# Optimization experiments

Measured on AMD Instinct MI355X. Metric: run time of the kernel, lower is better.

Reference implementation:

```python
import jax, jax.numpy as jnp
import numpy as np

BITS = 4
GROUP = 128
IN_F = 4096
OUT_F = 11008
N_GROUPS = IN_F // GROUP  # padded_in == in_features here


def fwht(v):
    """Orthonormal fast Walsh-Hadamard transform over the last axis (len = power of 2)."""
    orig = v.shape
    g = orig[-1]
    x = v.reshape(-1, g)
    h = 1
    while h < g:
        x = x.reshape(-1, g // (2 * h), 2, h)
        a, b = x[:, :, 0, :], x[:, :, 1, :]
        x = jnp.stack([a + b, a - b], axis=2).reshape(-1, g)
        h *= 2
    return (x * (1.0 / np.sqrt(g))).reshape(orig)


def setup_inputs() -> dict:
    key = jax.random.key(0)
    ks = jax.random.split(key, 7)
    x = jax.random.normal(ks[0], (4096, IN_F), dtype=jnp.float32)
    # packed 4-bit indices: two per byte, stored as int32 byte values
    packed_weight = jax.random.randint(ks[1], (OUT_F, IN_F // 2), 0, 256, dtype=jnp.int32)
    # per-(row, group) scale factors (positive)
    norms = jax.random.uniform(ks[2], (OUT_F, N_GROUPS), dtype=jnp.float32) * 0.1 + 0.01
    # Lloyd-Max codebook: 2^bits sorted centroids
    centroids = jnp.sort(jax.random.normal(ks[3], (2 ** BITS,), dtype=jnp.float32))
    # Rademacher sign vectors for the two-round signed WHT rotation
    signs1 = jnp.where(jax.random.normal(ks[4], (GROUP,)) >= 0, 1.0, -1.0).astype(jnp.float32)
    signs2 = jnp.where(jax.random.normal(ks[5], (GROUP,)) >= 0, 1.0, -1.0).astype(jnp.float32)
    bias = jax.random.normal(ks[6], (OUT_F,), dtype=jnp.float32) * 0.01
    return {"x": x, "packed_weight": packed_weight, "norms": norms,
            "centroids": centroids, "signs1": signs1, "signs2": signs2, "bias": bias}


def dequantize(packed_weight, norms, centroids, signs1, signs2):
    out_f, n_groups = norms.shape
    # unpack 4-bit nibbles: low nibble at even positions, high nibble at odd
    pw = packed_weight.astype(jnp.uint8)
    lo = (pw & 15).astype(jnp.int32)
    hi = (pw >> 4).astype(jnp.int32)
    idx = jnp.stack([lo, hi], axis=-1).reshape(out_f, -1)      # [out, padded_in]
    c = centroids[idx].reshape(out_f, n_groups, GROUP)          # codebook lookup
    # inverse of rotate(v) = H(s2 * H(s1 * v)):  v = s1 * H(s2 * H(u))
    u = fwht(c) * signs2
    u = fwht(u) * signs1
    w = u * norms[:, :, None]                                   # per-group rescale
    return w.reshape(out_f, -1)


def reference(x, packed_weight, norms, centroids, signs1, signs2, bias):
    w = dequantize(packed_weight, norms, centroids, signs1, signs2)[:, : x.shape[-1]]
    return x @ w.T + bias
```

## Files before the change

### kernel.cpp

```cpp
#include <hip/hip_runtime.h>
#include <stdint.h>

#define M_DIM 4096
#define K_DIM 4096
#define N_DIM 11008
#define N_GROUPS 32

typedef __attribute__((ext_vector_type(8))) short short8;
typedef __attribute__((ext_vector_type(4))) float floatx4;

__device__ __forceinline__ unsigned short f32_to_bf16(float f) {
    unsigned int u = __float_as_uint(f);
    unsigned int rounding = 0x7FFFu + ((u >> 16) & 1u);
    return (unsigned short)((u + rounding) >> 16);
}

__global__ __launch_bounds__(128) void make_M_kernel(
    const float* __restrict__ signs1, const float* __restrict__ signs2,
    unsigned short* __restrict__ Mt)
{
    const int i = blockIdx.x;
    const int j = threadIdx.x;
    __shared__ float s2s[128];
    s2s[j] = signs2[j];
    __syncthreads();
    float acc = 0.f;
#pragma unroll 8
    for (int a = 0; a < 128; ++a) {
        int par = (__popc(i & a) + __popc(a & j)) & 1;
        acc += par ? -s2s[a] : s2s[a];
    }
    Mt[i * 128 + j] = f32_to_bf16(signs1[j] * acc * (1.0f / 128.0f));
}

#define TX_RS 136

__global__ __launch_bounds__(256) void transform_x_kernel(
    const float* __restrict__ x,
    const unsigned short* __restrict__ Mt,
    unsigned short* __restrict__ z)
{
    __shared__ __align__(16) short Xs[64 * TX_RS];
    __shared__ __align__(16) short Ms[128 * TX_RS];

    const int tid = threadIdx.x;
    const int wave = tid >> 6, lane = tid & 63;
    const int col16 = lane & 15, quad = lane >> 4;
    const int m0 = (blockIdx.x >> 5) * 64;
    const int g = blockIdx.x & 31;
    const int c0 = g * 128;

#pragma unroll
    for (int it = 0; it < 8; ++it) {
        int idx = tid + 256 * it;
        int row = idx >> 5, c4 = idx & 31;
        float4 v = *(const float4*)(x + (size_t)(m0 + row) * K_DIM + c0 + c4 * 4);
        uint2 o;
        o.x = (unsigned)f32_to_bf16(v.x) | ((unsigned)f32_to_bf16(v.y) << 16);
        o.y = (unsigned)f32_to_bf16(v.z) | ((unsigned)f32_to_bf16(v.w) << 16);
        *(uint2*)(Xs + row * TX_RS + c4 * 4) = o;
    }
#pragma unroll
    for (int it = 0; it < 8; ++it) {
        int ch = tid + 256 * it;
        int row = ch >> 4, cc = ch & 15;
        uint4 v = *(const uint4*)(Mt + (size_t)ch * 8);
        *(uint4*)(Ms + row * TX_RS + cc * 8) = v;
    }
    __syncthreads();

    floatx4 acc[8] = {};
#pragma unroll
    for (int ks = 0; ks < 4; ++ks) {
        short8 af = *(const short8*)(Xs + (wave * 16 + col16) * TX_RS + ks * 32 + quad * 8);
#pragma unroll
        for (int ni = 0; ni < 8; ++ni) {
            short8 bf = *(const short8*)(Ms + (ni * 16 + col16) * TX_RS + ks * 32 + quad * 8);
            acc[ni] = __builtin_amdgcn_mfma_f32_16x16x32_bf16(af, bf, acc[ni], 0, 0, 0);
        }
    }
#pragma unroll
    for (int ni = 0; ni < 8; ++ni)
#pragma unroll
        for (int r = 0; r < 4; ++r) {
            int row = m0 + wave * 16 + quad * 4 + r;
            z[(size_t)row * K_DIM + c0 + ni * 16 + col16] = f32_to_bf16(acc[ni][r]);
        }
}

__global__ __launch_bounds__(256) void dequant_lut_kernel(
    const int* __restrict__ packed,
    const float* __restrict__ norms,
    const float* __restrict__ centroids,
    unsigned int* __restrict__ w_out)
{
    __shared__ float2 lut[256];
    const int tid = threadIdx.x;
    lut[tid] = make_float2(centroids[tid & 15], centroids[tid >> 4]);
    __syncthreads();

    const int row = blockIdx.x;
    const int g = tid >> 3;
    const float nrm = norms[row * N_GROUPS + g];
    const int* prow = packed + (size_t)row * 2048 + tid * 8;
    int4 pa = *(const int4*)(prow);
    int4 pb = *(const int4*)(prow + 4);
    int v[8] = {pa.x, pa.y, pa.z, pa.w, pb.x, pb.y, pb.z, pb.w};
    unsigned o[8];
#pragma unroll
    for (int q = 0; q < 8; ++q) {
        float2 c = lut[v[q] & 255];
        o[q] = (unsigned)f32_to_bf16(c.x * nrm) | ((unsigned)f32_to_bf16(c.y * nrm) << 16);
    }
    unsigned* orow = w_out + (size_t)row * 2048 + tid * 8;
    *(uint4*)(orow)     = make_uint4(o[0], o[1], o[2], o[3]);
    *(uint4*)(orow + 4) = make_uint4(o[4], o[5], o[6], o[7]);
}

#define BM 128
#define BN 128
#define BK 64
#define SMEM_BYTES 33792

typedef const __attribute__((address_space(1))) void* gvp_t;
typedef __attribute__((address_space(3))) void* svp_t;

__global__ __launch_bounds__(256, 4) void gemm_bt_kernel(
    const unsigned short* __restrict__ A,
    const unsigned short* __restrict__ B,
    const float* __restrict__ bias,
    float* __restrict__ C)
{
    __shared__ __align__(16) char smem[SMEM_BYTES];
    short* AsS = (short*)smem;
    short* BsS = (short*)(smem + 16384);

    const int tid = threadIdx.x;
    const int wave = tid >> 6, lane = tid & 63;
    const int wm = wave >> 1, wn = wave & 1;
    const int col16 = lane & 15, quad = lane >> 4;

    int id = blockIdx.x;
    int panel = id / 688;
    int rem = id - panel * 688;
    int nt = rem >> 3;
    int mt = panel * 8 + (rem & 7);
    const int m0 = mt * BM, n0 = nt * BN;

    const int srow = (lane >> 3);
    const int gc = (lane & 7) ^ srow;
    const unsigned short* aPtr = A + (size_t)(m0 + wave * 32 + srow) * K_DIM + gc * 8;
    const unsigned short* bPtr = B + (size_t)(n0 + wave * 32 + srow) * K_DIM + gc * 8;

    floatx4 acc[4][4] = {};

    const int nk = K_DIM / BK;
    for (int kt = 0; kt < nk; ++kt) {
        __syncthreads();
#pragma unroll
        for (int i = 0; i < 4; ++i) {
            __builtin_amdgcn_global_load_lds(
                (gvp_t)(aPtr + (size_t)i * 8 * K_DIM + kt * BK),
                (svp_t)(AsS + (wave * 4 + i) * 512), 16, 0, 0);
            __builtin_amdgcn_global_load_lds(
                (gvp_t)(bPtr + (size_t)i * 8 * K_DIM + kt * BK),
                (svp_t)(BsS + (wave * 4 + i) * 512), 16, 0, 0);
        }
        __syncthreads();

#pragma unroll
        for (int ks = 0; ks < BK / 32; ++ks) {
            const int cl = ((ks * 4 + quad) ^ (col16 & 7)) * 8;
            short8 af[4], bf[4];
#pragma unroll
            for (int mi = 0; mi < 4; ++mi) {
                af[mi] = *(const short8*)(AsS + (wm * 64 + mi * 16 + col16) * BK + cl);
                bf[mi] = *(const short8*)(BsS + (wn * 64 + mi * 16 + col16) * BK + cl);
            }
#pragma unroll
            for (int mi = 0; mi < 4; ++mi)
#pragma unroll
                for (int ni = 0; ni < 4; ++ni)
                    acc[mi][ni] = __builtin_amdgcn_mfma_f32_16x16x32_bf16(
                        af[mi], bf[ni], acc[mi][ni], 0, 0, 0);
        }
    }

    float bv[4];
#pragma unroll
    for (int ni = 0; ni < 4; ++ni) bv[ni] = bias[n0 + wn * 64 + ni * 16 + col16];

    float* Cs = (float*)smem;
#pragma unroll
    for (int s = 0; s < 2; ++s) {
        __syncthreads();
        if (wm == s) {
#pragma unroll
            for (int mi = 0; mi < 4; ++mi)
#pragma unroll
                for (int ni = 0; ni < 4; ++ni)
#pragma unroll
                    for (int r = 0; r < 4; ++r)
                        Cs[(mi * 16 + quad * 4 + r) * 132 + wn * 64 + ni * 16 + col16] =
                            acc[mi][ni][r] + bv[ni];
        }
        __syncthreads();
#pragma unroll
        for (int p = 0; p < 8; ++p) {
            int rr = p * 8 + (tid >> 5);
            int c4 = (tid & 31) * 4;
            floatx4 v = *(const floatx4*)(Cs + rr * 132 + c4);
            __builtin_nontemporal_store(v,
                (floatx4*)(C + (size_t)(m0 + s * 64 + rr) * N_DIM + n0 + c4));
        }
    }
}

extern "C" void kernel_launch(void* const* d_in, const int* in_sizes, int n_in,
                              void* d_out, int out_size, void* d_ws, size_t ws_size,
                              hipStream_t stream) {
    const float* x        = (const float*)d_in[0];
    const int* packed     = (const int*)d_in[1];
    const float* norms    = (const float*)d_in[2];
    const float* centroids= (const float*)d_in[3];
    const float* signs1   = (const float*)d_in[4];
    const float* signs2   = (const float*)d_in[5];
    const float* bias     = (const float*)d_in[6];
    float* out            = (float*)d_out;

    unsigned short* Mt     = (unsigned short*)d_ws;
    unsigned short* w_bf16 = (unsigned short*)((char*)d_ws + 32768);
    unsigned short* z_bf16 = (unsigned short*)((char*)d_ws + 32768 + (size_t)N_DIM * K_DIM * 2);

    make_M_kernel<<<128, 128, 0, stream>>>(signs1, signs2, Mt);

    transform_x_kernel<<<(M_DIM / 64) * N_GROUPS, 256, 0, stream>>>(x, Mt, z_bf16);

    dequant_lut_kernel<<<N_DIM, 256, 0, stream>>>(
        packed, norms, centroids, (unsigned int*)w_bf16);

    gemm_bt_kernel<<<dim3((N_DIM / BN) * (M_DIM / BM)), 256, 0, stream>>>(
        z_bf16, w_bf16, bias, out);
}
```

Measured before the change: 715.9 us.

## Rewrite GEMM as 256x256 tile, 8-wave double-buffered pipelined kernel

Replaces the 128x128 single-buffered GEMM with a 256x256 tile, 512-thread kernel. It double-buffers LDS through async global_load_lds and interleaves quarter-tile staging with MFMA phases using explicit waitcnt, barriers and setprio. Block-to-tile mapping is now XCD-aware, and the epilogue writes directly from registers instead of staging through LDS. The aim is to hide global load latency and raise arithmetic intensity. The cost is 128KB of LDS, heavy register use, and uncoalesced direct stores of the output.

```diff
diff --git a/kernel.cpp b/kernel.cpp
--- a/kernel.cpp
+++ b/kernel.cpp
@@ -117,103 +117,205 @@
     *(uint4*)(orow + 4) = make_uint4(o[4], o[5], o[6], o[7]);
 }
 
-#define BM 128
-#define BN 128
+#define BM 256
+#define BN 256
 #define BK 64
-#define SMEM_BYTES 33792
 
 typedef const __attribute__((address_space(1))) void* gvp_t;
 typedef __attribute__((address_space(3))) void* svp_t;
 
-__global__ __launch_bounds__(256, 4) void gemm_bt_kernel(
+#define GFENCE() asm volatile("" ::: "memory")
+#define BARRIER() do { GFENCE(); __builtin_amdgcn_s_barrier(); GFENCE(); } while (0)
+#define LGKM0() asm volatile("s_waitcnt lgkmcnt(0)" ::: "memory")
+#define LGKM8() asm volatile("s_waitcnt lgkmcnt(8)" ::: "memory")
+#define VM6()   asm volatile("s_waitcnt vmcnt(6)" ::: "memory")
+#define VM4()   asm volatile("s_waitcnt vmcnt(4)" ::: "memory")
+#define VM0()   asm volatile("s_waitcnt vmcnt(0)" ::: "memory")
+#define PRIO1() __builtin_amdgcn_s_setprio(1)
+#define PRIO0() __builtin_amdgcn_s_setprio(0)
+
+__device__ __forceinline__ void read_a4(short8 (&dst)[4][2], const short* rb, int s0) {
+#pragma unroll
+    for (int fm = 0; fm < 4; ++fm) {
+        dst[fm][0] = *(const short8*)(rb + fm * 1024 + s0);
+        dst[fm][1] = *(const short8*)(rb + fm * 1024 + (s0 ^ 32));
+    }
+}
+__device__ __forceinline__ void read_b2(short8 (&dst)[2][2], const short* rb, int s0) {
+#pragma unroll
+    for (int fn = 0; fn < 2; ++fn) {
+        dst[fn][0] = *(const short8*)(rb + fn * 1024 + s0);
+        dst[fn][1] = *(const short8*)(rb + fn * 1024 + (s0 ^ 32));
+    }
+}
+__device__ __forceinline__ void mfma_q(floatx4 (&acc)[4][2],
+                                       const short8 (&a)[4][2], const short8 (&b)[2][2]) {
+#pragma unroll
+    for (int ks = 0; ks < 2; ++ks)
+#pragma unroll
+        for (int fm = 0; fm < 4; ++fm)
+#pragma unroll
+            for (int fn = 0; fn < 2; ++fn)
+                acc[fm][fn] = __builtin_amdgcn_mfma_f32_16x16x32_bf16(
+                    a[fm][ks], b[fn][ks], acc[fm][fn], 0, 0, 0);
+}
+
+__global__ __launch_bounds__(512, 2) void gemm_bt_kernel(
     const unsigned short* __restrict__ A,
     const unsigned short* __restrict__ B,
     const float* __restrict__ bias,
     float* __restrict__ C)
 {
-    __shared__ __align__(16) char smem[SMEM_BYTES];
-    short* AsS = (short*)smem;
-    short* BsS = (short*)(smem + 16384);
+    __shared__ __align__(16) short smem[65536];
+    short* As = smem;
+    short* Bs = smem + 32768;
 
     const int tid = threadIdx.x;
-    const int wave = tid >> 6, lane = tid & 63;
-    const int wm = wave >> 1, wn = wave & 1;
+    const int w = tid >> 6, lane = tid & 63;
+    const int wm = w >> 2, wn = w & 3;
     const int col16 = lane & 15, quad = lane >> 4;
 
-    int id = blockIdx.x;
-    int panel = id / 688;
-    int rem = id - panel * 688;
-    int nt = rem >> 3;
-    int mt = panel * 8 + (rem & 7);
+    const int bid = blockIdx.x;
+    const int xcd = bid & 7, idx = bid >> 3;
+    const int mt = xcd * 2 + (idx & 1);
+    const int nt = idx >> 1;
     const int m0 = mt * BM, n0 = nt * BN;
 
-    const int srow = (lane >> 3);
-    const int gc = (lane & 7) ^ srow;
-    const unsigned short* aPtr = A + (size_t)(m0 + wave * 32 + srow) * K_DIM + gc * 8;
-    const unsigned short* bPtr = B + (size_t)(n0 + wave * 32 + srow) * K_DIM + gc * 8;
-
-    floatx4 acc[4][4] = {};
-
-    const int nk = K_DIM / BK;
-    for (int kt = 0; kt < nk; ++kt) {
-        __syncthreads();
-#pragma unroll
-        for (int i = 0; i < 4; ++i) {
-            __builtin_amdgcn_global_load_lds(
-                (gvp_t)(aPtr + (size_t)i * 8 * K_DIM + kt * BK),
-                (svp_t)(AsS + (wave * 4 + i) * 512), 16, 0, 0);
-            __builtin_amdgcn_global_load_lds(
-                (gvp_t)(bPtr + (size_t)i * 8 * K_DIM + kt * BK),
-                (svp_t)(BsS + (wave * 4 + i) * 512), 16, 0, 0);
-        }
-        __syncthreads();
-
-#pragma unroll
-        for (int ks = 0; ks < BK / 32; ++ks) {
-            const int cl = ((ks * 4 + quad) ^ (col16 & 7)) * 8;
-            short8 af[4], bf[4];
-#pragma unroll
-            for (int mi = 0; mi < 4; ++mi) {
-                af[mi] = *(const short8*)(AsS + (wm * 64 + mi * 16 + col16) * BK + cl);
-                bf[mi] = *(const short8*)(BsS + (wn * 64 + mi * 16 + col16) * BK + cl);
+    const int gc = (lane & 7) ^ (lane >> 3);
+    const unsigned short* aSrc = A + (size_t)(m0 + w * 8 + (lane >> 3)) * K_DIM + gc * 8;
+    const unsigned short* bSrc = B + (size_t)(n0 + (w >> 2) * 64 + (w & 3) * 8 + (lane >> 3)) * K_DIM + gc * 8;
+    const int wOff = w * 512;
+
+#define STAGE_A(BUF, H, KT) do { \
+    __builtin_amdgcn_global_load_lds((gvp_t)(aSrc + (size_t)((H) * 64) * K_DIM + (KT) * 64), \
+        (svp_t)(As + (BUF) * 16384 + (H) * 8192 + wOff), 16, 0, 0); \
+    __builtin_amdgcn_global_load_lds((gvp_t)(aSrc + (size_t)((H) * 64 + 128) * K_DIM + (KT) * 64), \
+        (svp_t)(As + (BUF) * 16384 + (H) * 8192 + 4096 + wOff), 16, 0, 0); \
+} while (0)
+#define STAGE_B(BUF, H, KT) do { \
+    __builtin_amdgcn_global_load_lds((gvp_t)(bSrc + (size_t)((H) * 32) * K_DIM + (KT) * 64), \
+        (svp_t)(Bs + (BUF) * 16384 + (H) * 8192 + wOff), 16, 0, 0); \
+    __builtin_amdgcn_global_load_lds((gvp_t)(bSrc + (size_t)((H) * 32 + 128) * K_DIM + (KT) * 64), \
+        (svp_t)(Bs + (BUF) * 16384 + (H) * 8192 + 4096 + wOff), 16, 0, 0); \
+} while (0)
+
+    const short* aR = As + (wm * 64 + col16) * 64;
+    const short* bR = Bs + (wn * 32 + col16) * 64;
+    const int s0 = (quad ^ (col16 & 7)) << 3;
+
+    short8 a0[4][2], a1[4][2], b0[2][2], b1[2][2];
+    floatx4 acc[2][2][4][2];
+#pragma unroll
+    for (int i0 = 0; i0 < 2; ++i0)
+#pragma unroll
+        for (int i1 = 0; i1 < 2; ++i1)
+#pragma unroll
+            for (int i2 = 0; i2 < 4; ++i2)
+#pragma unroll
+                for (int i3 = 0; i3 < 2; ++i3)
+                    acc[i0][i1][i2][i3] = (floatx4)0.0f;
+
+    STAGE_A(0, 0, 0); STAGE_B(0, 0, 0); STAGE_A(0, 1, 0); STAGE_B(0, 1, 0);
+    VM4();
+    STAGE_A(1, 0, 1); STAGE_B(1, 0, 1); STAGE_A(1, 1, 1);
+    VM6();
+    BARRIER();
+
+    const int NIT = K_DIM / (2 * BK) - 1;
+    for (int i = 0; i < NIT; ++i) {
+        const int t = 2 * i;
+        read_a4(a0, aR, s0); read_b2(b0, bR, s0);
+        STAGE_B(1, 1, t + 1);
+        LGKM8();
+        BARRIER(); LGKM0();
+        PRIO1(); mfma_q(acc[0][0], a0, b0); PRIO0();
+        BARRIER();
+        read_a4(a1, aR + 8192, s0);
+        STAGE_A(0, 0, t + 2);
+        BARRIER(); LGKM0();
+        PRIO1(); mfma_q(acc[1][0], a1, b0); PRIO0();
+        BARRIER();
+        read_b2(b1, bR + 8192, s0);
+        STAGE_B(0, 0, t + 2);
+        BARRIER(); LGKM0();
+        PRIO1(); mfma_q(acc[0][1], a0, b1); PRIO0();
+        BARRIER();
+        STAGE_A(0, 1, t + 2);
+        VM6();
+        BARRIER();
+        PRIO1(); mfma_q(acc[1][1], a1, b1); PRIO0();
+        BARRIER();
+        read_a4(a0, aR + 16384, s0); read_b2(b0, bR + 16384, s0);
+        STAGE_B(0, 1, t + 2);
+        LGKM8();
+        BARRIER(); LGKM0();
+        PRIO1(); mfma_q(acc[0][0], a0, b0); PRIO0();
+        BARRIER();
+        read_a4(a1, aR + 16384 + 8192, s0);
+        STAGE_A(1, 0, t + 3);
+        BARRIER(); LGKM0();
+        PRIO1(); mfma_q(acc[1][0], a1, b0); PRIO0();
+        BARRIER();
+        read_b2(b1, bR + 16384 + 8192, s0);
+        STAGE_B(1, 0, t + 3);
+        BARRIER(); LGKM0();
+        PRIO1(); mfma_q(acc[0][1], a0, b1); PRIO0();
+        BARRIER();
+        STAGE_A(1, 1, t + 3);
+        VM6();
+        BARRIER();
+        PRIO1(); mfma_q(acc[1][1], a1, b1); PRIO0();
+        BARRIER();
+    }
+
+    read_a4(a0, aR, s0); read_b2(b0, bR, s0);
+    STAGE_B(1, 1, 63);
+    BARRIER(); LGKM0();
+    mfma_q(acc[0][0], a0, b0);
+    BARRIER();
+    read_a4(a1, aR + 8192, s0);
+    BARRIER(); LGKM0();
+    mfma_q(acc[1][0], a1, b0);
+    BARRIER();
+    read_b2(b1, bR + 8192, s0);
+    BARRIER(); LGKM0();
+    mfma_q(acc[0][1], a0, b1);
+    BARRIER();
+    VM0();
+    BARRIER();
+    mfma_q(acc[1][1], a1, b1);
+    read_a4(a0, aR + 16384, s0); read_b2(b0, bR + 16384, s0);
+    mfma_q(acc[0][0], a0, b0);
+    read_a4(a1, aR + 16384 + 8192, s0);
+    mfma_q(acc[1][0], a1, b0);
+    read_b2(b1, bR + 16384 + 8192, s0);
+    mfma_q(acc[0][1], a0, b1);
+    mfma_q(acc[1][1], a1, b1);
+
+#undef STAGE_A
+#undef STAGE_B
+
+    float bv[2][2];
+#pragma unroll
+    for (int qn = 0; qn < 2; ++qn)
+#pragma unroll
+        for (int fn = 0; fn < 2; ++fn)
+            bv[qn][fn] = bias[n0 + wn * 64 + qn * 32 + fn * 16 + col16];
+
+#pragma unroll
+    for (int qm = 0; qm < 2; ++qm)
+#pragma unroll
+        for (int fm = 0; fm < 4; ++fm)
+#pragma unroll
+            for (int r = 0; r < 4; ++r) {
+                float* crow = C + (size_t)(m0 + wm * 128 + qm * 64 + fm * 16 + quad * 4 + r) * N_DIM
+                              + n0 + wn * 64 + col16;
+#pragma unroll
+                for (int qn = 0; qn < 2; ++qn)
+#pragma unroll
+                    for (int fn = 0; fn < 2; ++fn)
+                        crow[qn * 32 + fn * 16] = acc[qm][qn][fm][fn][r] + bv[qn][fn];
             }
-#pragma unroll
-            for (int mi = 0; mi < 4; ++mi)
-#pragma unroll
-                for (int ni = 0; ni < 4; ++ni)
-                    acc[mi][ni] = __builtin_amdgcn_mfma_f32_16x16x32_bf16(
-                        af[mi], bf[ni], acc[mi][ni], 0, 0, 0);
-        }
-    }
-
-    float bv[4];
-#pragma unroll
-    for (int ni = 0; ni < 4; ++ni) bv[ni] = bias[n0 + wn * 64 + ni * 16 + col16];
-
-    float* Cs = (float*)smem;
-#pragma unroll
-    for (int s = 0; s < 2; ++s) {
-        __syncthreads();
-        if (wm == s) {
-#pragma unroll
-            for (int mi = 0; mi < 4; ++mi)
-#pragma unroll
-                for (int ni = 0; ni < 4; ++ni)
-#pragma unroll
-                    for (int r = 0; r < 4; ++r)
-                        Cs[(mi * 16 + quad * 4 + r) * 132 + wn * 64 + ni * 16 + col16] =
-                            acc[mi][ni][r] + bv[ni];
-        }
-        __syncthreads();
-#pragma unroll
-        for (int p = 0; p < 8; ++p) {
-            int rr = p * 8 + (tid >> 5);
-            int c4 = (tid & 31) * 4;
-            floatx4 v = *(const floatx4*)(Cs + rr * 132 + c4);
-            __builtin_nontemporal_store(v,
-                (floatx4*)(C + (size_t)(m0 + s * 64 + rr) * N_DIM + n0 + c4));
-        }
-    }
 }
 
 extern "C" void kernel_launch(void* const* d_in, const int* in_sizes, int n_in,
@@ -239,6 +341,6 @@
     dequant_lut_kernel<<<N_DIM, 256, 0, stream>>>(
         packed, norms, centroids, (unsigned int*)w_bf16);
 
-    gemm_bt_kernel<<<dim3((N_DIM / BN) * (M_DIM / BM)), 256, 0, stream>>>(
+    gemm_bt_kernel<<<dim3((M_DIM / BM) * (N_DIM / BN)), 512, 0, stream>>>(
         z_bf16, w_bf16, bias, out);
 }
```

Result: faster. 600.0 us (-16.2%).
